# Kernel optimization log

Hardware: AMD Instinct MI355X
Metric: run time of the kernel (lower is better)

Reference implementation:

```python
import jax, jax.numpy as jnp
import numpy as np

N, K, D = 65536, 64, 128
ALPHA = 1.0

def setup_inputs() -> dict:
    key = jax.random.key(0)
    k1, k2 = jax.random.split(key)
    z = jax.random.normal(k1, (N, D), dtype=jnp.float32)
    centroids = jax.random.normal(k2, (K, D), dtype=jnp.float32)
    return {"z": z, "centroids": centroids}

def reference(z, centroids):
    # squared euclidean distance per (sample, cluster): sum over feature dim
    diff = jnp.sum((z[:, None, :] - centroids[None, :, :]) ** 2, axis=2)  # [N, K]
    numerator = 1.0 / (1.0 + diff / ALPHA)
    power = (ALPHA + 1.0) / 2.0
    numerator = numerator ** power
    q = numerator / jnp.sum(numerator, axis=1, keepdims=True)  # row-normalized soft assignment
    return q
```

## Files before the change

### kernel.cpp

```cpp
#include <hip/hip_runtime.h>
#include <hip/hip_bf16.h>


using bf16x8 = __attribute__((ext_vector_type(8))) __bf16;
using f32x4  = __attribute__((ext_vector_type(4))) float;

constexpr int K_CL = 64;
constexpr int D_FT = 128;
constexpr int CSTR = 136;

__global__ __launch_bounds__(256) void cluster_assign_mfma(
    const float* __restrict__ z,
    const float* __restrict__ cent,
    float* __restrict__ out)
{
    __shared__ __bf16 c_bf[K_CL * CSTR];
    __shared__ float  b_lds[K_CL];

    const int tid  = threadIdx.x;
    const int wave = tid >> 6;
    const int lane = tid & 63;
    const int lo   = lane & 15;
    const int g    = lane >> 4;

    {
        const float4* c4 = reinterpret_cast<const float4*>(cent);
        #pragma unroll
        for (int i = 0; i < 8; ++i) {
            int f   = tid + i * 256;
            int row = f >> 5;
            int c4i = f & 31;
            float4 v = c4[f];
            __bf16* dst = &c_bf[row * CSTR + c4i * 4];
            dst[0] = (__bf16)v.x; dst[1] = (__bf16)v.y;
            dst[2] = (__bf16)v.z; dst[3] = (__bf16)v.w;
        }
        if (tid < K_CL) b_lds[tid] = 1.0f;
    }
    __syncthreads();

    {
        int c = tid & 63, q = tid >> 6;
        const float4* p = reinterpret_cast<const float4*>(cent + c * D_FT + q * 32);
        float s = 0.f;
        #pragma unroll
        for (int j = 0; j < 8; ++j) {
            float4 v = p[j];
            s = fmaf(v.x, v.x, s); s = fmaf(v.y, v.y, s);
            s = fmaf(v.z, v.z, s); s = fmaf(v.w, v.w, s);
        }
        __hip_atomic_fetch_add(&b_lds[c], s,
                               __ATOMIC_RELAXED, __HIP_MEMORY_SCOPE_WORKGROUP);
    }

    bf16x8 bf[4][4];
    #pragma unroll
    for (int nt = 0; nt < 4; ++nt)
        #pragma unroll
        for (int kk = 0; kk < 4; ++kk)
            bf[nt][kk] = *reinterpret_cast<const bf16x8*>(
                &c_bf[(lo + nt * 16) * CSTR + kk * 32 + g * 8]);

    __syncthreads();

    float bmine[4];
    #pragma unroll
    for (int nt = 0; nt < 4; ++nt) bmine[nt] = b_lds[lo + nt * 16];

    for (int it = 0; it < 2; ++it) {
        const int rowbase = blockIdx.x * 128 + it * 64 + wave * 16;

        const char* zb = reinterpret_cast<const char*>(z)
                       + (size_t)(rowbase + lo) * 512 + g * 32;
        float4 zst[8];
        #pragma unroll
        for (int kk = 0; kk < 4; ++kk) {
            zst[2*kk]   = *reinterpret_cast<const float4*>(zb + kk * 128);
            zst[2*kk+1] = *reinterpret_cast<const float4*>(zb + kk * 128 + 16);
        }

        float zn = 0.f;
        #pragma unroll
        for (int j = 0; j < 8; ++j) {
            float4 v = zst[j];
            zn = fmaf(v.x, v.x, zn); zn = fmaf(v.y, v.y, zn);
            zn = fmaf(v.z, v.z, zn); zn = fmaf(v.w, v.w, zn);
        }
        zn += __shfl_xor(zn, 16);
        zn += __shfl_xor(zn, 32);

        bf16x8 af[4];
        #pragma unroll
        for (int kk = 0; kk < 4; ++kk) {
            float4 u = zst[2*kk], v = zst[2*kk+1];
            bf16x8 a;
            a[0] = (__bf16)u.x; a[1] = (__bf16)u.y;
            a[2] = (__bf16)u.z; a[3] = (__bf16)u.w;
            a[4] = (__bf16)v.x; a[5] = (__bf16)v.y;
            a[6] = (__bf16)v.z; a[7] = (__bf16)v.w;
            af[kk] = a;
        }

        f32x4 acc[4] = {{0,0,0,0},{0,0,0,0},{0,0,0,0},{0,0,0,0}};
        #pragma unroll
        for (int kk = 0; kk < 4; ++kk)
            #pragma unroll
            for (int nt = 0; nt < 4; ++nt)
                acc[nt] = __builtin_amdgcn_mfma_f32_16x16x32_bf16(
                              af[kk], bf[nt][kk], acc[nt], 0, 0, 0);

        float znr[4];
        #pragma unroll
        for (int r = 0; r < 4; ++r) znr[r] = __shfl(zn, g * 4 + r);

        float num[4][4];
        float psum[4] = {0.f, 0.f, 0.f, 0.f};
        #pragma unroll
        for (int nt = 0; nt < 4; ++nt)
            #pragma unroll
            for (int r = 0; r < 4; ++r) {
                float d1 = fmaf(-2.f, acc[nt][r], znr[r] + bmine[nt]);
                float nv = __builtin_amdgcn_rcpf(d1);
                num[nt][r] = nv;
                psum[r] += nv;
            }
        #pragma unroll
        for (int r = 0; r < 4; ++r) {
            psum[r] += __shfl_xor(psum[r], 1);
            psum[r] += __shfl_xor(psum[r], 2);
            psum[r] += __shfl_xor(psum[r], 4);
            psum[r] += __shfl_xor(psum[r], 8);
            psum[r] = __builtin_amdgcn_rcpf(psum[r]);
        }

        #pragma unroll
        for (int nt = 0; nt < 4; ++nt)
            #pragma unroll
            for (int r = 0; r < 4; ++r)
                out[(size_t)(rowbase + g * 4 + r) * K_CL + lo + nt * 16]
                    = num[nt][r] * psum[r];
    }
}

extern "C" void kernel_launch(void* const* d_in, const int* in_sizes, int n_in,
                              void* d_out, int out_size, void* d_ws, size_t ws_size,
                              hipStream_t stream) {
    const float* z    = (const float*)d_in[0];
    const float* cent = (const float*)d_in[1];
    float* out        = (float*)d_out;

    dim3 grid(65536 / 128);
    cluster_assign_mfma<<<grid, dim3(256), 0, stream>>>(z, cent, out);
}
```

Measured before the change: 79.36 us.

## Precompute bf16 centroids and norms in a prep kernel, drop LDS staging

Adds a single-block prep kernel that converts the centroids to bf16 and computes their squared norms plus one into workspace. The main kernel no longer stages centroids in LDS, so it has no block-wide syncs or atomics and reads B fragments directly from global memory (cache-resident). Each block now handles 64 rows instead of looping over 128, which doubles the grid. The cost is an extra kernel launch and serialization on the tiny prep kernel, plus repeated global/L2 reads of B fragments inside the MFMA loop.

```diff
diff --git a/kernel.cpp b/kernel.cpp
--- a/kernel.cpp
+++ b/kernel.cpp
@@ -7,139 +7,126 @@
 
 constexpr int K_CL = 64;
 constexpr int D_FT = 128;
-constexpr int CSTR = 136;
+
+__global__ __launch_bounds__(256) void prep_kernel(
+    const float* __restrict__ cent,
+    __bf16* __restrict__ cb,
+    float* __restrict__ bv)
+{
+    const int t = threadIdx.x;
+    const int c = t >> 2, q = t & 3;
+    const float4* p = reinterpret_cast<const float4*>(cent + c * D_FT + q * 32);
+    bf16x8* dst = reinterpret_cast<bf16x8*>(cb + c * D_FT + q * 32);
+    float s = 0.f;
+    #pragma unroll
+    for (int h = 0; h < 4; ++h) {
+        float4 u = p[2 * h], v = p[2 * h + 1];
+        s = fmaf(u.x, u.x, s); s = fmaf(u.y, u.y, s);
+        s = fmaf(u.z, u.z, s); s = fmaf(u.w, u.w, s);
+        s = fmaf(v.x, v.x, s); s = fmaf(v.y, v.y, s);
+        s = fmaf(v.z, v.z, s); s = fmaf(v.w, v.w, s);
+        bf16x8 a;
+        a[0] = (__bf16)u.x; a[1] = (__bf16)u.y;
+        a[2] = (__bf16)u.z; a[3] = (__bf16)u.w;
+        a[4] = (__bf16)v.x; a[5] = (__bf16)v.y;
+        a[6] = (__bf16)v.z; a[7] = (__bf16)v.w;
+        dst[h] = a;
+    }
+    s += __shfl_xor(s, 1);
+    s += __shfl_xor(s, 2);
+    if (q == 0) bv[c] = 1.f + s;
+}
 
 __global__ __launch_bounds__(256) void cluster_assign_mfma(
     const float* __restrict__ z,
-    const float* __restrict__ cent,
+    const __bf16* __restrict__ cb,
+    const float* __restrict__ bv,
     float* __restrict__ out)
 {
-    __shared__ __bf16 c_bf[K_CL * CSTR];
-    __shared__ float  b_lds[K_CL];
-
     const int tid  = threadIdx.x;
     const int wave = tid >> 6;
     const int lane = tid & 63;
     const int lo   = lane & 15;
     const int g    = lane >> 4;
 
-    {
-        const float4* c4 = reinterpret_cast<const float4*>(cent);
-        #pragma unroll
-        for (int i = 0; i < 8; ++i) {
-            int f   = tid + i * 256;
-            int row = f >> 5;
-            int c4i = f & 31;
-            float4 v = c4[f];
-            __bf16* dst = &c_bf[row * CSTR + c4i * 4];
-            dst[0] = (__bf16)v.x; dst[1] = (__bf16)v.y;
-            dst[2] = (__bf16)v.z; dst[3] = (__bf16)v.w;
-        }
-        if (tid < K_CL) b_lds[tid] = 1.0f;
-    }
-    __syncthreads();
+    const int rowbase = blockIdx.x * 64 + wave * 16;
 
-    {
-        int c = tid & 63, q = tid >> 6;
-        const float4* p = reinterpret_cast<const float4*>(cent + c * D_FT + q * 32);
-        float s = 0.f;
-        #pragma unroll
-        for (int j = 0; j < 8; ++j) {
-            float4 v = p[j];
-            s = fmaf(v.x, v.x, s); s = fmaf(v.y, v.y, s);
-            s = fmaf(v.z, v.z, s); s = fmaf(v.w, v.w, s);
-        }
-        __hip_atomic_fetch_add(&b_lds[c], s,
-                               __ATOMIC_RELAXED, __HIP_MEMORY_SCOPE_WORKGROUP);
+    const char* zb = reinterpret_cast<const char*>(z)
+                   + (size_t)(rowbase + lo) * 512 + g * 32;
+    float4 zst[8];
+    #pragma unroll
+    for (int kk = 0; kk < 4; ++kk) {
+        zst[2*kk]   = *reinterpret_cast<const float4*>(zb + kk * 128);
+        zst[2*kk+1] = *reinterpret_cast<const float4*>(zb + kk * 128 + 16);
     }
 
-    bf16x8 bf[4][4];
+    float bmine[4];
+    #pragma unroll
+    for (int nt = 0; nt < 4; ++nt) bmine[nt] = bv[lo + nt * 16];
+
+    float zn = 0.f;
+    #pragma unroll
+    for (int j = 0; j < 8; ++j) {
+        float4 v = zst[j];
+        zn = fmaf(v.x, v.x, zn); zn = fmaf(v.y, v.y, zn);
+        zn = fmaf(v.z, v.z, zn); zn = fmaf(v.w, v.w, zn);
+    }
+    zn += __shfl_xor(zn, 16);
+    zn += __shfl_xor(zn, 32);
+
+    bf16x8 af[4];
+    #pragma unroll
+    for (int kk = 0; kk < 4; ++kk) {
+        float4 u = zst[2*kk], v = zst[2*kk+1];
+        bf16x8 a;
+        a[0] = (__bf16)u.x; a[1] = (__bf16)u.y;
+        a[2] = (__bf16)u.z; a[3] = (__bf16)u.w;
+        a[4] = (__bf16)v.x; a[5] = (__bf16)v.y;
+        a[6] = (__bf16)v.z; a[7] = (__bf16)v.w;
+        af[kk] = a;
+    }
+
+    f32x4 acc[4] = {{0,0,0,0},{0,0,0,0},{0,0,0,0},{0,0,0,0}};
+    #pragma unroll
+    for (int kk = 0; kk < 4; ++kk)
+        #pragma unroll
+        for (int nt = 0; nt < 4; ++nt) {
+            bf16x8 b = *reinterpret_cast<const bf16x8*>(
+                cb + (lo + nt * 16) * D_FT + kk * 32 + g * 8);
+            acc[nt] = __builtin_amdgcn_mfma_f32_16x16x32_bf16(
+                          af[kk], b, acc[nt], 0, 0, 0);
+        }
+
+    float znr[4];
+    #pragma unroll
+    for (int r = 0; r < 4; ++r) znr[r] = __shfl(zn, g * 4 + r);
+
+    float num[4][4];
+    float psum[4] = {0.f, 0.f, 0.f, 0.f};
     #pragma unroll
     for (int nt = 0; nt < 4; ++nt)
         #pragma unroll
-        for (int kk = 0; kk < 4; ++kk)
-            bf[nt][kk] = *reinterpret_cast<const bf16x8*>(
-                &c_bf[(lo + nt * 16) * CSTR + kk * 32 + g * 8]);
+        for (int r = 0; r < 4; ++r) {
+            float d1 = fmaf(-2.f, acc[nt][r], znr[r] + bmine[nt]);
+            float nv = __builtin_amdgcn_rcpf(d1);
+            num[nt][r] = nv;
+            psum[r] += nv;
+        }
+    #pragma unroll
+    for (int r = 0; r < 4; ++r) {
+        psum[r] += __shfl_xor(psum[r], 1);
+        psum[r] += __shfl_xor(psum[r], 2);
+        psum[r] += __shfl_xor(psum[r], 4);
+        psum[r] += __shfl_xor(psum[r], 8);
+        psum[r] = __builtin_amdgcn_rcpf(psum[r]);
+    }
 
-    __syncthreads();
-
-    float bmine[4];
     #pragma unroll
-    for (int nt = 0; nt < 4; ++nt) bmine[nt] = b_lds[lo + nt * 16];
-
-    for (int it = 0; it < 2; ++it) {
-        const int rowbase = blockIdx.x * 128 + it * 64 + wave * 16;
-
-        const char* zb = reinterpret_cast<const char*>(z)
-                       + (size_t)(rowbase + lo) * 512 + g * 32;
-        float4 zst[8];
+    for (int nt = 0; nt < 4; ++nt)
         #pragma unroll
-        for (int kk = 0; kk < 4; ++kk) {
-            zst[2*kk]   = *reinterpret_cast<const float4*>(zb + kk * 128);
-            zst[2*kk+1] = *reinterpret_cast<const float4*>(zb + kk * 128 + 16);
-        }
-
-        float zn = 0.f;
-        #pragma unroll
-        for (int j = 0; j < 8; ++j) {
-            float4 v = zst[j];
-            zn = fmaf(v.x, v.x, zn); zn = fmaf(v.y, v.y, zn);
-            zn = fmaf(v.z, v.z, zn); zn = fmaf(v.w, v.w, zn);
-        }
-        zn += __shfl_xor(zn, 16);
-        zn += __shfl_xor(zn, 32);
-
-        bf16x8 af[4];
-        #pragma unroll
-        for (int kk = 0; kk < 4; ++kk) {
-            float4 u = zst[2*kk], v = zst[2*kk+1];
-            bf16x8 a;
-            a[0] = (__bf16)u.x; a[1] = (__bf16)u.y;
-            a[2] = (__bf16)u.z; a[3] = (__bf16)u.w;
-            a[4] = (__bf16)v.x; a[5] = (__bf16)v.y;
-            a[6] = (__bf16)v.z; a[7] = (__bf16)v.w;
-            af[kk] = a;
-        }
-
-        f32x4 acc[4] = {{0,0,0,0},{0,0,0,0},{0,0,0,0},{0,0,0,0}};
-        #pragma unroll
-        for (int kk = 0; kk < 4; ++kk)
-            #pragma unroll
-            for (int nt = 0; nt < 4; ++nt)
-                acc[nt] = __builtin_amdgcn_mfma_f32_16x16x32_bf16(
-                              af[kk], bf[nt][kk], acc[nt], 0, 0, 0);
-
-        float znr[4];
-        #pragma unroll
-        for (int r = 0; r < 4; ++r) znr[r] = __shfl(zn, g * 4 + r);
-
-        float num[4][4];
-        float psum[4] = {0.f, 0.f, 0.f, 0.f};
-        #pragma unroll
-        for (int nt = 0; nt < 4; ++nt)
-            #pragma unroll
-            for (int r = 0; r < 4; ++r) {
-                float d1 = fmaf(-2.f, acc[nt][r], znr[r] + bmine[nt]);
-                float nv = __builtin_amdgcn_rcpf(d1);
-                num[nt][r] = nv;
-                psum[r] += nv;
-            }
-        #pragma unroll
-        for (int r = 0; r < 4; ++r) {
-            psum[r] += __shfl_xor(psum[r], 1);
-            psum[r] += __shfl_xor(psum[r], 2);
-            psum[r] += __shfl_xor(psum[r], 4);
-            psum[r] += __shfl_xor(psum[r], 8);
-            psum[r] = __builtin_amdgcn_rcpf(psum[r]);
-        }
-
-        #pragma unroll
-        for (int nt = 0; nt < 4; ++nt)
-            #pragma unroll
-            for (int r = 0; r < 4; ++r)
-                out[(size_t)(rowbase + g * 4 + r) * K_CL + lo + nt * 16]
-                    = num[nt][r] * psum[r];
-    }
+        for (int r = 0; r < 4; ++r)
+            out[(size_t)(rowbase + g * 4 + r) * K_CL + lo + nt * 16]
+                = num[nt][r] * psum[r];
 }
 
 extern "C" void kernel_launch(void* const* d_in, const int* in_sizes, int n_in,
@@ -149,6 +136,9 @@
     const float* cent = (const float*)d_in[1];
     float* out        = (float*)d_out;
 
-    dim3 grid(65536 / 128);
-    cluster_assign_mfma<<<grid, dim3(256), 0, stream>>>(z, cent, out);
+    __bf16* cb = (__bf16*)d_ws;
+    float*  bv = (float*)((char*)d_ws + 16384);
+
+    prep_kernel<<<dim3(1), dim3(256), 0, stream>>>(cent, cb, bv);
+    cluster_assign_mfma<<<dim3(65536 / 64), dim3(256), 0, stream>>>(z, cb, bv, out);
 }
```

New measurement: 90.64 us. 1.14x slower.
